# Kernel tuning notes

Hardware: AMD Instinct MI355X
Metric: run time of the kernel (lower is better)

The kernel has to match this reference:

```python
import jax, jax.numpy as jnp
import numpy as np

N0, N1, N2, N3 = 600000, 100000, 10000, 1000
E0, E1, E2 = 1000000, 100000, 10000
DIN, DH, DOUT = 128, 256, 47


def _glorot(k, fan_in, fan_out):
    s = np.sqrt(2.0 / (fan_in + fan_out)).astype(np.float32)
    return jax.random.normal(k, (fan_in, fan_out), jnp.float32) * s


def setup_inputs() -> dict:
    key = jax.random.key(0)
    ks = jax.random.split(key, 13)
    return {
        "x": jax.random.normal(ks[0], (N0, DIN), jnp.float32),
        "src0": jax.random.randint(ks[1], (E0,), 0, N0, jnp.int32),
        "dst0": jax.random.randint(ks[2], (E0,), 0, N1, jnp.int32),
        "src1": jax.random.randint(ks[3], (E1,), 0, N1, jnp.int32),
        "dst1": jax.random.randint(ks[4], (E1,), 0, N2, jnp.int32),
        "src2": jax.random.randint(ks[5], (E2,), 0, N2, jnp.int32),
        "dst2": jax.random.randint(ks[6], (E2,), 0, N3, jnp.int32),
        "Wl0": _glorot(ks[7], DIN, DH), "Wr0": _glorot(ks[8], DIN, DH),
        "b0": jnp.zeros((DH,), jnp.float32),
        "Wl1": _glorot(ks[9], DH, DH), "Wr1": _glorot(ks[10], DH, DH),
        "b1": jnp.zeros((DH,), jnp.float32),
        "Wl2": _glorot(ks[11], DH, DOUT), "Wr2": _glorot(ks[12], DH, DOUT),
        "b2": jnp.zeros((DOUT,), jnp.float32),
        "size1": N1, "size2": N2, "size3": N3,
    }


def _sage_conv(x, src, dst, n_tgt, Wl, Wr, b):
    # PyG SAGEConv (mean aggr, root_weight=True, bias in lin_l) on a bipartite
    # sampled subgraph: x_src = x (all frontier nodes), x_tgt = x[:n_tgt].
    msgs = x[src]                                   # [E, Din] gather
    agg = jax.ops.segment_sum(msgs, dst, num_segments=n_tgt)
    cnt = jax.ops.segment_sum(jnp.ones((dst.shape[0],), x.dtype), dst,
                              num_segments=n_tgt)
    mean = agg / jnp.maximum(cnt, 1.0)[:, None]     # [n_tgt, Din]
    return mean @ Wl + b + x[:n_tgt] @ Wr           # [n_tgt, Dout]


def reference(x, src0, dst0, src1, dst1, src2, dst2,
              Wl0, Wr0, b0, Wl1, Wr1, b1, Wl2, Wr2, b2,
              size1, size2, size3):
    # layer 0
    h = jax.nn.relu(_sage_conv(x, src0, dst0, size1, Wl0, Wr0, b0))
    # dropout(p=0.5) is identity in eval mode
    # layer 1
    h = jax.nn.relu(_sage_conv(h, src1, dst1, size2, Wl1, Wr1, b1))
    # layer 2 (no relu/dropout)
    h = _sage_conv(h, src2, dst2, size3, Wl2, Wr2, b2)
    return jax.nn.log_softmax(h, axis=-1)           # [size3, out_channels]
```

## Files before the change

kernel.cpp:

```cpp
#include <hip/hip_runtime.h>
#include <hip/hip_bf16.h>
#include <cstdint>
#include <cstddef>
#include <cmath>

#define N0C 600000
#define N1C 100000
#define N2C 10000
#define N3C 1000
#define E0C 1000000
#define E1C 100000
#define E2C 10000

typedef unsigned short u16;
typedef unsigned int u32;
typedef __attribute__((ext_vector_type(8))) short bf16x8;
typedef __attribute__((ext_vector_type(4))) float f32x4;

__device__ __forceinline__ u16 f2b(float x) {
  u32 u = __builtin_bit_cast(u32, x);
  u32 r = (u + 0x7fffu + ((u >> 16) & 1u)) >> 16;
  return (u16)r;
}
__device__ __forceinline__ u16 f2b_hw(float x) {
  __hip_bfloat16 h = __float2bfloat16(x);
  u16 r;
  __builtin_memcpy(&r, &h, 2);
  return r;
}
__device__ __forceinline__ float b2f(u16 h) {
  u32 u = ((u32)h) << 16;
  return __builtin_bit_cast(float, u);
}

__global__ __launch_bounds__(256) void hist3(
    const int* __restrict__ d0, const int* __restrict__ d1,
    const int* __restrict__ d2, const int* __restrict__ s1,
    int* __restrict__ c0, int* __restrict__ c1, int* __restrict__ c2,
    int* __restrict__ f) {
  int i = blockIdx.x * blockDim.x + threadIdx.x;
  if (i < E0C) {
    atomicAdd(&c0[d0[i]], 1);
    if (i < N2C) f[i] = 1;
  } else if (i < E0C + E1C) {
    int j = i - E0C;
    atomicAdd(&c1[d1[j]], 1);
    f[s1[j]] = 1;
  } else if (i < E0C + E1C + E2C) {
    atomicAdd(&c2[d2[i - E0C - E1C]], 1);
  }
}

__global__ __launch_bounds__(256) void scan_block3(
    int* __restrict__ c0, int* __restrict__ c1, int* __restrict__ c2,
    int* __restrict__ f, int* __restrict__ p0, int* __restrict__ p1,
    int* __restrict__ p2, int* __restrict__ pf) {
  __shared__ int sdata[256];
  const int b = blockIdx.x;
  int* data; int n; int* partials; int lb;
  if (b < 98)       { data = c0; n = N1C; partials = p0; lb = b; }
  else if (b < 108) { data = c1; n = N2C; partials = p1; lb = b - 98; }
  else if (b < 109) { data = c2; n = N3C; partials = p2; lb = b - 108; }
  else              { data = f;  n = N1C; partials = pf; lb = b - 109; }
  const int t = threadIdx.x;
  const int idx = lb * 1024 + t * 4;
  int v[4];
  int sum = 0;
#pragma unroll
  for (int k = 0; k < 4; k++) {
    int x = (idx + k < n) ? data[idx + k] : 0;
    v[k] = x; sum += x;
  }
  sdata[t] = sum;
  __syncthreads();
  for (int off = 1; off < 256; off <<= 1) {
    int x = (t >= off) ? sdata[t - off] : 0;
    __syncthreads();
    sdata[t] += x;
    __syncthreads();
  }
  int run = (t > 0) ? sdata[t - 1] : 0;
#pragma unroll
  for (int k = 0; k < 4; k++) {
    run += v[k];
    if (idx + k < n) data[idx + k] = run;
  }
  if (t == 255) partials[lb] = sdata[255];
}

__global__ __launch_bounds__(128) void scan_partials3(
    int* __restrict__ p0, int* __restrict__ p1, int* __restrict__ p2,
    int* __restrict__ pf) {
  __shared__ int sdata[128];
  int* p; int nb;
  if (blockIdx.x == 0)      { p = p0; nb = 98; }
  else if (blockIdx.x == 1) { p = p1; nb = 10; }
  else if (blockIdx.x == 2) { p = p2; nb = 1; }
  else                      { p = pf; nb = 98; }
  const int t = threadIdx.x;
  sdata[t] = (t < nb) ? p[t] : 0;
  __syncthreads();
  for (int off = 1; off < 128; off <<= 1) {
    int x = (t >= off) ? sdata[t - off] : 0;
    __syncthreads();
    sdata[t] += x;
    __syncthreads();
  }
  int ex = (t > 0) ? sdata[t - 1] : 0;
  if (t < nb) p[t] = ex;
}

__global__ __launch_bounds__(256) void addoff3(
    const int* __restrict__ c0, const int* __restrict__ c1,
    const int* __restrict__ c2, const int* __restrict__ p0,
    const int* __restrict__ p1, const int* __restrict__ p2,
    int* __restrict__ o0, int* __restrict__ o1, int* __restrict__ o2,
    const int* __restrict__ f, const int* __restrict__ pf,
    int* __restrict__ cidx, int* __restrict__ list,
    int* __restrict__ cnt_need) {
  int i = blockIdx.x * blockDim.x + threadIdx.x;
  if (i < N1C) {
    o0[i + 1] = c0[i] + p0[i >> 10];
    if (i == 0) o0[0] = 0;
    int F = f[i] + pf[i >> 10];
    int prev = (i > 0) ? (f[i - 1] + pf[(i - 1) >> 10]) : 0;
    cidx[i] = prev;
    if (F > prev) list[prev] = i;
    if (i == N1C - 1) cnt_need[0] = F;
  } else if (i < N1C + N2C) {
    int j = i - N1C;
    o1[j + 1] = c1[j] + p1[j >> 10];
    if (j == 0) o1[0] = 0;
  } else if (i < N1C + N2C + N3C) {
    int j = i - N1C - N2C;
    o2[j + 1] = c2[j] + p2[j >> 10];
    if (j == 0) o2[0] = 0;
  }
}

__global__ __launch_bounds__(256) void fill3(
    const int* __restrict__ s0, const int* __restrict__ d0,
    const int* __restrict__ s1, const int* __restrict__ d1,
    const int* __restrict__ s2, const int* __restrict__ d2,
    const int* __restrict__ o0, const int* __restrict__ o1,
    const int* __restrict__ o2, int* __restrict__ u0, int* __restrict__ u1,
    int* __restrict__ u2, int* __restrict__ e0, int* __restrict__ e1,
    int* __restrict__ e2, const int* __restrict__ cidx) {
  int i = blockIdx.x * blockDim.x + threadIdx.x;
  if (i < E0C) {
    int d = d0[i]; int p = atomicAdd(&u0[d], 1); e0[o0[d] + p] = s0[i];
  } else if (i < E0C + E1C) {
    int j = i - E0C;
    int d = d1[j]; int p = atomicAdd(&u1[d], 1);
    e1[o1[d] + p] = cidx[s1[j]];
  } else if (i < E0C + E1C + E2C) {
    int j = i - E0C - E1C;
    int d = d2[j]; int p = atomicAdd(&u2[d], 1); e2[o2[d] + p] = s2[j];
  }
}

__global__ __launch_bounds__(256) void cvt_wt2(
    const float* __restrict__ Wl0, const float* __restrict__ Wr0,
    const float* __restrict__ Wl1, const float* __restrict__ Wr1,
    u16* __restrict__ Wt0, u16* __restrict__ Wt1) {
  int idx = blockIdx.x * blockDim.x + threadIdx.x;
  if (idx < 256 * 256) {
    int n = idx >> 8, k = idx & 255;
    float v = (k < 128) ? Wl0[(size_t)k * 256 + n] : Wr0[(size_t)(k - 128) * 256 + n];
    Wt0[idx] = f2b(v);
  } else if (idx < 256 * 256 + 256 * 512) {
    int j = idx - 256 * 256;
    int n = j >> 9, k = j & 511;
    float v = (k < 256) ? Wl1[(size_t)k * 256 + n] : Wr1[(size_t)(k - 256) * 256 + n];
    Wt1[j] = f2b(v);
  }
}

__global__ __launch_bounds__(256) void gather128_f32(
    const float* __restrict__ X, const int* __restrict__ off,
    const int* __restrict__ esrc, const int* __restrict__ list,
    const int* __restrict__ cnt_need, u16* __restrict__ mean) {
  int w = (blockIdx.x * blockDim.x + threadIdx.x) >> 6;
  int lane = threadIdx.x & 63;
  if (w >= cnt_need[0]) return;
  const int node = list[w];
  const int half = lane >> 5, l32 = lane & 31;
  int s = off[node], e = off[node + 1];
  float a0 = 0.f, a1 = 0.f, a2 = 0.f, a3 = 0.f;
  int j = s;
  for (; j + 3 < e; j += 4) {
    float4 v0 = *(const float4*)(X + (size_t)esrc[j + half] * 128 + l32 * 4);
    float4 v1 = *(const float4*)(X + (size_t)esrc[j + 2 + half] * 128 + l32 * 4);
    a0 += v0.x + v1.x; a1 += v0.y + v1.y;
    a2 += v0.z + v1.z; a3 += v0.w + v1.w;
  }
  for (; j + 1 < e; j += 2) {
    float4 v = *(const float4*)(X + (size_t)esrc[j + half] * 128 + l32 * 4);
    a0 += v.x; a1 += v.y; a2 += v.z; a3 += v.w;
  }
  if (j < e && half == 0) {
    float4 v = *(const float4*)(X + (size_t)esrc[j] * 128 + l32 * 4);
    a0 += v.x; a1 += v.y; a2 += v.z; a3 += v.w;
  }
  a0 += __shfl_xor(a0, 32, 64);
  a1 += __shfl_xor(a1, 32, 64);
  a2 += __shfl_xor(a2, 32, 64);
  a3 += __shfl_xor(a3, 32, 64);
  if (half == 0) {
    float inv = 1.0f / fmaxf((float)(e - s), 1.0f);
    uint2 pk;
    pk.x = ((u32)f2b(a1 * inv) << 16) | (u32)f2b(a0 * inv);
    pk.y = ((u32)f2b(a3 * inv) << 16) | (u32)f2b(a2 * inv);
    *(uint2*)(mean + (size_t)w * 128 + l32 * 4) = pk;
  }
}

__global__ __launch_bounds__(256) void gather256_bf16(
    const u16* __restrict__ X, const int* __restrict__ off,
    const int* __restrict__ esrc, int Nt, u16* __restrict__ mean) {
  int w = (blockIdx.x * blockDim.x + threadIdx.x) >> 6;
  int lane = threadIdx.x & 63;
  if (w >= Nt) return;
  int s = off[w], e = off[w + 1];
  float a0 = 0.f, a1 = 0.f, a2 = 0.f, a3 = 0.f;
  int j = s;
  for (; j + 3 < e; j += 4) {
    ushort4 v0 = *(const ushort4*)(X + (size_t)esrc[j + 0] * 256 + lane * 4);
    ushort4 v1 = *(const ushort4*)(X + (size_t)esrc[j + 1] * 256 + lane * 4);
    ushort4 v2 = *(const ushort4*)(X + (size_t)esrc[j + 2] * 256 + lane * 4);
    ushort4 v3 = *(const ushort4*)(X + (size_t)esrc[j + 3] * 256 + lane * 4);
    a0 += b2f(v0.x) + b2f(v1.x) + b2f(v2.x) + b2f(v3.x);
    a1 += b2f(v0.y) + b2f(v1.y) + b2f(v2.y) + b2f(v3.y);
    a2 += b2f(v0.z) + b2f(v1.z) + b2f(v2.z) + b2f(v3.z);
    a3 += b2f(v0.w) + b2f(v1.w) + b2f(v2.w) + b2f(v3.w);
  }
  for (; j < e; j++) {
    ushort4 v0 = *(const ushort4*)(X + (size_t)esrc[j] * 256 + lane * 4);
    a0 += b2f(v0.x); a1 += b2f(v0.y); a2 += b2f(v0.z); a3 += b2f(v0.w);
  }
  float inv = 1.0f / fmaxf((float)(e - s), 1.0f);
  ushort4 o;
  o.x = f2b(a0 * inv); o.y = f2b(a1 * inv); o.z = f2b(a2 * inv); o.w = f2b(a3 * inv);
  *(ushort4*)(mean + (size_t)w * 256 + lane * 4) = o;
}

__global__ __launch_bounds__(256) void gemm_mfma_l0(
    const u16* __restrict__ A1, const float* __restrict__ A2,
    const int* __restrict__ list, const int* __restrict__ cnt_need,
    const u16* __restrict__ Wt, const float* __restrict__ bias,
    u16* __restrict__ C) {
  const int M = cnt_need[0];
  if ((int)blockIdx.x * 128 >= M) return;
  const int tid = threadIdx.x;
  const int wave = tid >> 6, lane = tid & 63;
  const int lr = lane & 15, quad = lane >> 4;
  const int wr = wave >> 1, wc = wave & 1;
  const int rowBase = blockIdx.x * 128 + wr * 64;
  const int colBase = blockIdx.y * 128 + wc * 64;

  f32x4 acc[4][4] = {};

  int rrow[4], node[4];
#pragma unroll
  for (int mt = 0; mt < 4; mt++) {
    int r = rowBase + mt * 16 + lr;
    if (r >= M) r = M - 1;
    rrow[mt] = r;
    node[mt] = list[r];
  }
  const u16* wrow[4];
  float bs[4];
#pragma unroll
  for (int nt = 0; nt < 4; nt++) {
    int n = colBase + nt * 16 + lr;
    wrow[nt] = Wt + (size_t)n * 256;
    bs[nt] = bias[n];
  }

#pragma unroll
  for (int kt = 0; kt < 128; kt += 32) {
    bf16x8 af[4], bfr[4];
#pragma unroll
    for (int mt = 0; mt < 4; mt++)
      af[mt] = *(const bf16x8*)(A1 + (size_t)rrow[mt] * 128 + kt + quad * 8);
#pragma unroll
    for (int nt = 0; nt < 4; nt++)
      bfr[nt] = *(const bf16x8*)(wrow[nt] + kt + quad * 8);
#pragma unroll
    for (int mt = 0; mt < 4; mt++)
#pragma unroll
      for (int nt = 0; nt < 4; nt++)
        acc[mt][nt] = __builtin_amdgcn_mfma_f32_16x16x32_bf16(
            af[mt], bfr[nt], acc[mt][nt], 0, 0, 0);
  }
#pragma unroll
  for (int kt = 0; kt < 128; kt += 32) {
    bf16x8 af[4], bfr[4];
#pragma unroll
    for (int mt = 0; mt < 4; mt++) {
      const float* s = A2 + (size_t)node[mt] * 128 + kt + quad * 8;
      float4 v0 = *(const float4*)s;
      float4 v1 = *(const float4*)(s + 4);
      bf16x8 t;
      t[0] = (short)f2b_hw(v0.x); t[1] = (short)f2b_hw(v0.y);
      t[2] = (short)f2b_hw(v0.z); t[3] = (short)f2b_hw(v0.w);
      t[4] = (short)f2b_hw(v1.x); t[5] = (short)f2b_hw(v1.y);
      t[6] = (short)f2b_hw(v1.z); t[7] = (short)f2b_hw(v1.w);
      af[mt] = t;
    }
#pragma unroll
    for (int nt = 0; nt < 4; nt++)
      bfr[nt] = *(const bf16x8*)(wrow[nt] + 128 + kt + quad * 8);
#pragma unroll
    for (int mt = 0; mt < 4; mt++)
#pragma unroll
      for (int nt = 0; nt < 4; nt++)
        acc[mt][nt] = __builtin_amdgcn_mfma_f32_16x16x32_bf16(
            af[mt], bfr[nt], acc[mt][nt], 0, 0, 0);
  }

#pragma unroll
  for (int mt = 0; mt < 4; mt++) {
#pragma unroll
    for (int reg = 0; reg < 4; reg++) {
      int row = rowBase + mt * 16 + quad * 4 + reg;
      if (row < M) {
#pragma unroll
        for (int nt = 0; nt < 4; nt++) {
          float v = fmaxf(acc[mt][nt][reg] + bs[nt], 0.f);
          C[(size_t)row * 256 + colBase + nt * 16 + lr] = f2b(v);
        }
      }
    }
  }
}

__global__ __launch_bounds__(256) void gemm_mfma(
    const u16* __restrict__ A1, const u16* __restrict__ A2, int Kh,
    const u16* __restrict__ Wt, const float* __restrict__ bias,
    u16* __restrict__ C, int M, int do_relu) {
  const int tid = threadIdx.x;
  const int wave = tid >> 6, lane = tid & 63;
  const int lr = lane & 15, quad = lane >> 4;
  const int wr = wave >> 1, wc = wave & 1;
  const int rowBase = blockIdx.x * 128 + wr * 64;
  const int colBase = blockIdx.y * 128 + wc * 64;
  const int Ktot = 2 * Kh;

  f32x4 acc[4][4] = {};

  size_t aoff[4];
#pragma unroll
  for (int mt = 0; mt < 4; mt++) {
    int r = rowBase + mt * 16 + lr;
    if (r >= M) r = M - 1;
    aoff[mt] = (size_t)r * Kh;
  }
  const u16* wrow[4];
  float bs[4];
#pragma unroll
  for (int nt = 0; nt < 4; nt++) {
    int n = colBase + nt * 16 + lr;
    wrow[nt] = Wt + (size_t)n * Ktot;
    bs[nt] = bias[n];
  }

#pragma unroll
  for (int half = 0; half < 2; half++) {
    const u16* Asrc = half ? A2 : A1;
    const int kb = half * Kh;
    for (int kt = 0; kt < Kh; kt += 32) {
      bf16x8 af[4], bfr[4];
#pragma unroll
      for (int mt = 0; mt < 4; mt++)
        af[mt] = *(const bf16x8*)(Asrc + aoff[mt] + kt + quad * 8);
#pragma unroll
      for (int nt = 0; nt < 4; nt++)
        bfr[nt] = *(const bf16x8*)(wrow[nt] + kb + kt + quad * 8);
#pragma unroll
      for (int mt = 0; mt < 4; mt++)
#pragma unroll
        for (int nt = 0; nt < 4; nt++)
          acc[mt][nt] = __builtin_amdgcn_mfma_f32_16x16x32_bf16(
              af[mt], bfr[nt], acc[mt][nt], 0, 0, 0);
    }
  }

#pragma unroll
  for (int mt = 0; mt < 4; mt++) {
#pragma unroll
    for (int reg = 0; reg < 4; reg++) {
      int row = rowBase + mt * 16 + quad * 4 + reg;
      if (row < M) {
#pragma unroll
        for (int nt = 0; nt < 4; nt++) {
          float v = acc[mt][nt][reg] + bs[nt];
          if (do_relu) v = fmaxf(v, 0.f);
          C[(size_t)row * 256 + colBase + nt * 16 + lr] = f2b(v);
        }
      }
    }
  }
}

__global__ __launch_bounds__(64) void l2_fused(
    const u16* __restrict__ h2, const int* __restrict__ off,
    const int* __restrict__ esrc, const float* __restrict__ Wl2,
    const float* __restrict__ Wr2, const float* __restrict__ b2,
    float* __restrict__ out) {
  __shared__ float arow[512];
  const int i = blockIdx.x;
  const int lane = threadIdx.x;

  int s = off[i], e = off[i + 1];
  float a0 = 0.f, a1 = 0.f, a2 = 0.f, a3 = 0.f;
  int j = s;
  for (; j + 3 < e; j += 4) {
    ushort4 v0 = *(const ushort4*)(h2 + (size_t)esrc[j + 0] * 256 + lane * 4);
    ushort4 v1 = *(const ushort4*)(h2 + (size_t)esrc[j + 1] * 256 + lane * 4);
    ushort4 v2 = *(const ushort4*)(h2 + (size_t)esrc[j + 2] * 256 + lane * 4);
    ushort4 v3 = *(const ushort4*)(h2 + (size_t)esrc[j + 3] * 256 + lane * 4);
    a0 += b2f(v0.x) + b2f(v1.x) + b2f(v2.x) + b2f(v3.x);
    a1 += b2f(v0.y) + b2f(v1.y) + b2f(v2.y) + b2f(v3.y);
    a2 += b2f(v0.z) + b2f(v1.z) + b2f(v2.z) + b2f(v3.z);
    a3 += b2f(v0.w) + b2f(v1.w) + b2f(v2.w) + b2f(v3.w);
  }
  for (; j < e; j++) {
    ushort4 v0 = *(const ushort4*)(h2 + (size_t)esrc[j] * 256 + lane * 4);
    a0 += b2f(v0.x); a1 += b2f(v0.y); a2 += b2f(v0.z); a3 += b2f(v0.w);
  }
  float inv = 1.0f / fmaxf((float)(e - s), 1.0f);
  arow[lane * 4 + 0] = a0 * inv;
  arow[lane * 4 + 1] = a1 * inv;
  arow[lane * 4 + 2] = a2 * inv;
  arow[lane * 4 + 3] = a3 * inv;
  ushort4 r = *(const ushort4*)(h2 + (size_t)i * 256 + lane * 4);
  arow[256 + lane * 4 + 0] = b2f(r.x);
  arow[256 + lane * 4 + 1] = b2f(r.y);
  arow[256 + lane * 4 + 2] = b2f(r.z);
  arow[256 + lane * 4 + 3] = b2f(r.w);
  __syncthreads();

  float acc = 0.0f;
  if (lane < 47) {
    acc = b2[lane];
#pragma unroll 4
    for (int k = 0; k < 256; k++) acc += arow[k] * Wl2[k * 47 + lane];
#pragma unroll 4
    for (int k = 0; k < 256; k++) acc += arow[256 + k] * Wr2[k * 47 + lane];
  }
  float v = (lane < 47) ? acc : -INFINITY;
#pragma unroll
  for (int off2 = 32; off2 >= 1; off2 >>= 1) v = fmaxf(v, __shfl_xor(v, off2, 64));
  float e2 = (lane < 47) ? expf(acc - v) : 0.0f;
  float s2 = e2;
#pragma unroll
  for (int off2 = 32; off2 >= 1; off2 >>= 1) s2 += __shfl_xor(s2, off2, 64);
  if (lane < 47) out[(size_t)i * 47 + lane] = acc - v - logf(s2);
}

extern "C" void kernel_launch(void* const* d_in, const int* in_sizes, int n_in,
                              void* d_out, int out_size, void* d_ws, size_t ws_size,
                              hipStream_t stream) {
  (void)in_sizes; (void)n_in; (void)out_size; (void)ws_size;
  const float* x   = (const float*)d_in[0];
  const int* src0  = (const int*)d_in[1];
  const int* dst0  = (const int*)d_in[2];
  const int* src1  = (const int*)d_in[3];
  const int* dst1  = (const int*)d_in[4];
  const int* src2  = (const int*)d_in[5];
  const int* dst2  = (const int*)d_in[6];
  const float* Wl0 = (const float*)d_in[7];
  const float* Wr0 = (const float*)d_in[8];
  const float* b0  = (const float*)d_in[9];
  const float* Wl1 = (const float*)d_in[10];
  const float* Wr1 = (const float*)d_in[11];
  const float* b1  = (const float*)d_in[12];
  const float* Wl2 = (const float*)d_in[13];
  const float* Wr2 = (const float*)d_in[14];
  const float* b2  = (const float*)d_in[15];

  char* p = (char*)d_ws;
  u16* mean0 = (u16*)p; p += (size_t)N1C * 128 * 2;
  u16* h1    = (u16*)p; p += (size_t)N1C * 256 * 2;
  u16* mean1 = (u16*)p; p += (size_t)N2C * 256 * 2;
  u16* h2    = (u16*)p; p += (size_t)N2C * 256 * 2;
  u16* Wt0   = (u16*)p; p += (size_t)256 * 256 * 2;
  u16* Wt1   = (u16*)p; p += (size_t)256 * 512 * 2;
  int* cnt0  = (int*)p;
  int* cur0  = cnt0 + 100000;
  int* cnt1  = cur0 + 100000;
  int* cur1  = cnt1 + 10000;
  int* cnt2  = cur1 + 10000;
  int* cur2  = cnt2 + 1000;
  int* f     = cur2 + 1000;
  int* off0  = f + 100000 + 48;
  int* off1  = off0 + 100096;
  int* off2  = off1 + 10112;
  int* part0 = off2 + 1088;
  int* part1 = part0 + 128;
  int* part2 = part1 + 128;
  int* pf    = part2 + 128;
  int* cntN  = pf + 128;
  int* cidx  = cntN + 64;
  int* list  = cidx + 100000;
  int* esrc0 = list + 100000;
  int* esrc1 = esrc0 + 1000000;
  int* esrc2 = esrc1 + 100000;
  float* out = (float*)d_out;

  hipMemsetAsync(cnt0, 0, (size_t)322000 * 4, stream);
  hist3<<<(E0C + E1C + E2C + 255) / 256, 256, 0, stream>>>(
      dst0, dst1, dst2, src1, cnt0, cnt1, cnt2, f);
  scan_block3<<<207, 256, 0, stream>>>(cnt0, cnt1, cnt2, f,
                                       part0, part1, part2, pf);
  scan_partials3<<<4, 128, 0, stream>>>(part0, part1, part2, pf);
  addoff3<<<(N1C + N2C + N3C + 255) / 256, 256, 0, stream>>>(
      cnt0, cnt1, cnt2, part0, part1, part2, off0, off1, off2,
      f, pf, cidx, list, cntN);
  fill3<<<(E0C + E1C + E2C + 255) / 256, 256, 0, stream>>>(
      src0, dst0, src1, dst1, src2, dst2, off0, off1, off2,
      cur0, cur1, cur2, esrc0, esrc1, esrc2, cidx);

  cvt_wt2<<<(256 * 256 + 256 * 512 + 255) / 256, 256, 0, stream>>>(
      Wl0, Wr0, Wl1, Wr1, Wt0, Wt1);

  gather128_f32<<<N1C / 4, 256, 0, stream>>>(x, off0, esrc0, list, cntN, mean0);
  gemm_mfma_l0<<<dim3(782, 2), 256, 0, stream>>>(mean0, x, list, cntN,
                                                 Wt0, b0, h1);

  gather256_bf16<<<N2C / 4, 256, 0, stream>>>(h1, off1, esrc1, N2C, mean1);
  gemm_mfma<<<dim3(79, 2), 256, 0, stream>>>(mean1, h1, 256, Wt1, b1, h2, N2C, 1);

  l2_fused<<<N3C, 64, 0, stream>>>(h2, off2, esrc2, Wl2, Wr2, b2, out);
}
```

Baseline: 696.7 us.

## Fold partial scans into addoff, compact frontier via atomics, merge weight conversion

Removes the scan_partials3 kernel by redoing the small partial-sum scan in shared memory inside addoff3. The frontier-node scan is replaced by an atomic counter that assigns compact ids to needed nodes beyond the first N2C. The weight conversion kernel is merged into fill3, and the layer-0 gather loop is unrolled to 8 edges per iteration. This cuts two kernel launches plus the frontier scan work, at the cost of a nondeterministic compaction order that changes the row order of the mean0 and h1 buffers.

```diff
diff --git a/kernel.cpp b/kernel.cpp
--- a/kernel.cpp
+++ b/kernel.cpp
@@ -37,11 +37,11 @@
     const int* __restrict__ d0, const int* __restrict__ d1,
     const int* __restrict__ d2, const int* __restrict__ s1,
     int* __restrict__ c0, int* __restrict__ c1, int* __restrict__ c2,
-    int* __restrict__ f) {
+    int* __restrict__ f, int* __restrict__ cntN) {
   int i = blockIdx.x * blockDim.x + threadIdx.x;
+  if (i == 0) cntN[0] = N2C;
   if (i < E0C) {
     atomicAdd(&c0[d0[i]], 1);
-    if (i < N2C) f[i] = 1;
   } else if (i < E0C + E1C) {
     int j = i - E0C;
     atomicAdd(&c1[d1[j]], 1);
@@ -53,15 +53,13 @@
 
 __global__ __launch_bounds__(256) void scan_block3(
     int* __restrict__ c0, int* __restrict__ c1, int* __restrict__ c2,
-    int* __restrict__ f, int* __restrict__ p0, int* __restrict__ p1,
-    int* __restrict__ p2, int* __restrict__ pf) {
+    int* __restrict__ p0, int* __restrict__ p1, int* __restrict__ p2) {
   __shared__ int sdata[256];
   const int b = blockIdx.x;
   int* data; int n; int* partials; int lb;
   if (b < 98)       { data = c0; n = N1C; partials = p0; lb = b; }
   else if (b < 108) { data = c1; n = N2C; partials = p1; lb = b - 98; }
-  else if (b < 109) { data = c2; n = N3C; partials = p2; lb = b - 108; }
-  else              { data = f;  n = N1C; partials = pf; lb = b - 109; }
+  else              { data = c2; n = N3C; partials = p2; lb = b - 108; }
   const int t = threadIdx.x;
   const int idx = lb * 1024 + t * 4;
   int v[4];
@@ -88,52 +86,46 @@
   if (t == 255) partials[lb] = sdata[255];
 }
 
-__global__ __launch_bounds__(128) void scan_partials3(
-    int* __restrict__ p0, int* __restrict__ p1, int* __restrict__ p2,
-    int* __restrict__ pf) {
-  __shared__ int sdata[128];
-  int* p; int nb;
-  if (blockIdx.x == 0)      { p = p0; nb = 98; }
-  else if (blockIdx.x == 1) { p = p1; nb = 10; }
-  else if (blockIdx.x == 2) { p = p2; nb = 1; }
-  else                      { p = pf; nb = 98; }
-  const int t = threadIdx.x;
-  sdata[t] = (t < nb) ? p[t] : 0;
-  __syncthreads();
-  for (int off = 1; off < 128; off <<= 1) {
-    int x = (t >= off) ? sdata[t - off] : 0;
-    __syncthreads();
-    sdata[t] += x;
-    __syncthreads();
-  }
-  int ex = (t > 0) ? sdata[t - 1] : 0;
-  if (t < nb) p[t] = ex;
-}
-
 __global__ __launch_bounds__(256) void addoff3(
     const int* __restrict__ c0, const int* __restrict__ c1,
     const int* __restrict__ c2, const int* __restrict__ p0,
-    const int* __restrict__ p1, const int* __restrict__ p2,
+    const int* __restrict__ p1,
     int* __restrict__ o0, int* __restrict__ o1, int* __restrict__ o2,
-    const int* __restrict__ f, const int* __restrict__ pf,
-    int* __restrict__ cidx, int* __restrict__ list,
-    int* __restrict__ cnt_need) {
-  int i = blockIdx.x * blockDim.x + threadIdx.x;
+    const int* __restrict__ f, int* __restrict__ cidx,
+    int* __restrict__ list, int* __restrict__ cntN) {
+  __shared__ int sp0[128];
+  __shared__ int sp1[16];
+  const int t = threadIdx.x;
+  if (t < 128) sp0[t] = (t < 98) ? p0[t] : 0;
+  if (t >= 128 && t < 144) sp1[t - 128] = ((t - 128) < 10) ? p1[t - 128] : 0;
+  __syncthreads();
+  for (int off = 1; off < 128; off <<= 1) {
+    int x0 = (t < 128 && t >= off) ? sp0[t - off] : 0;
+    int x1 = (t >= 128 && t < 144 && (t - 128) >= off) ? sp1[t - 128 - off] : 0;
+    __syncthreads();
+    if (t < 128) sp0[t] += x0;
+    if (t >= 128 && t < 144) sp1[t - 128] += x1;
+    __syncthreads();
+  }
+  int i = blockIdx.x * blockDim.x + t;
   if (i < N1C) {
-    o0[i + 1] = c0[i] + p0[i >> 10];
+    int q = i >> 10;
+    o0[i + 1] = c0[i] + (q ? sp0[q - 1] : 0);
     if (i == 0) o0[0] = 0;
-    int F = f[i] + pf[i >> 10];
-    int prev = (i > 0) ? (f[i - 1] + pf[(i - 1) >> 10]) : 0;
-    cidx[i] = prev;
-    if (F > prev) list[prev] = i;
-    if (i == N1C - 1) cnt_need[0] = F;
+    if (i < N2C) {
+      cidx[i] = i; list[i] = i;
+    } else if (f[i]) {
+      int id = atomicAdd(cntN, 1);
+      cidx[i] = id; list[id] = i;
+    }
   } else if (i < N1C + N2C) {
     int j = i - N1C;
-    o1[j + 1] = c1[j] + p1[j >> 10];
+    int q = j >> 10;
+    o1[j + 1] = c1[j] + (q ? sp1[q - 1] : 0);
     if (j == 0) o1[0] = 0;
   } else if (i < N1C + N2C + N3C) {
     int j = i - N1C - N2C;
-    o2[j + 1] = c2[j] + p2[j >> 10];
+    o2[j + 1] = c2[j];
     if (j == 0) o2[0] = 0;
   }
 }
@@ -145,7 +137,10 @@
     const int* __restrict__ o0, const int* __restrict__ o1,
     const int* __restrict__ o2, int* __restrict__ u0, int* __restrict__ u1,
     int* __restrict__ u2, int* __restrict__ e0, int* __restrict__ e1,
-    int* __restrict__ e2, const int* __restrict__ cidx) {
+    int* __restrict__ e2, const int* __restrict__ cidx,
+    const float* __restrict__ Wl0, const float* __restrict__ Wr0,
+    const float* __restrict__ Wl1, const float* __restrict__ Wr1,
+    u16* __restrict__ Wt0, u16* __restrict__ Wt1) {
   int i = blockIdx.x * blockDim.x + threadIdx.x;
   if (i < E0C) {
     int d = d0[i]; int p = atomicAdd(&u0[d], 1); e0[o0[d] + p] = s0[i];
@@ -156,23 +151,20 @@
   } else if (i < E0C + E1C + E2C) {
     int j = i - E0C - E1C;
     int d = d2[j]; int p = atomicAdd(&u2[d], 1); e2[o2[d] + p] = s2[j];
-  }
-}
-
-__global__ __launch_bounds__(256) void cvt_wt2(
-    const float* __restrict__ Wl0, const float* __restrict__ Wr0,
-    const float* __restrict__ Wl1, const float* __restrict__ Wr1,
-    u16* __restrict__ Wt0, u16* __restrict__ Wt1) {
-  int idx = blockIdx.x * blockDim.x + threadIdx.x;
-  if (idx < 256 * 256) {
-    int n = idx >> 8, k = idx & 255;
-    float v = (k < 128) ? Wl0[(size_t)k * 256 + n] : Wr0[(size_t)(k - 128) * 256 + n];
-    Wt0[idx] = f2b(v);
-  } else if (idx < 256 * 256 + 256 * 512) {
-    int j = idx - 256 * 256;
-    int n = j >> 9, k = j & 511;
-    float v = (k < 256) ? Wl1[(size_t)k * 256 + n] : Wr1[(size_t)(k - 256) * 256 + n];
-    Wt1[j] = f2b(v);
+  } else {
+    int k = i - (E0C + E1C + E2C);
+    if (k < 256 * 256) {
+      int n = k >> 8, kk = k & 255;
+      float v = (kk < 128) ? Wl0[(size_t)kk * 256 + n]
+                           : Wr0[(size_t)(kk - 128) * 256 + n];
+      Wt0[k] = f2b(v);
+    } else if (k < 256 * 256 + 256 * 512) {
+      int j = k - 256 * 256;
+      int n = j >> 9, kk = j & 511;
+      float v = (kk < 256) ? Wl1[(size_t)kk * 256 + n]
+                           : Wr1[(size_t)(kk - 256) * 256 + n];
+      Wt1[j] = f2b(v);
+    }
   }
 }
 
@@ -188,11 +180,15 @@
   int s = off[node], e = off[node + 1];
   float a0 = 0.f, a1 = 0.f, a2 = 0.f, a3 = 0.f;
   int j = s;
-  for (; j + 3 < e; j += 4) {
+  for (; j + 7 < e; j += 8) {
     float4 v0 = *(const float4*)(X + (size_t)esrc[j + half] * 128 + l32 * 4);
     float4 v1 = *(const float4*)(X + (size_t)esrc[j + 2 + half] * 128 + l32 * 4);
-    a0 += v0.x + v1.x; a1 += v0.y + v1.y;
-    a2 += v0.z + v1.z; a3 += v0.w + v1.w;
+    float4 v2 = *(const float4*)(X + (size_t)esrc[j + 4 + half] * 128 + l32 * 4);
+    float4 v3 = *(const float4*)(X + (size_t)esrc[j + 6 + half] * 128 + l32 * 4);
+    a0 += v0.x + v1.x + v2.x + v3.x;
+    a1 += v0.y + v1.y + v2.y + v3.y;
+    a2 += v0.z + v1.z + v2.z + v3.z;
+    a3 += v0.w + v1.w + v2.w + v3.w;
   }
   for (; j + 1 < e; j += 2) {
     float4 v = *(const float4*)(X + (size_t)esrc[j + half] * 128 + l32 * 4);
@@ -500,8 +496,7 @@
   int* part0 = off2 + 1088;
   int* part1 = part0 + 128;
   int* part2 = part1 + 128;
-  int* pf    = part2 + 128;
-  int* cntN  = pf + 128;
+  int* cntN  = part2 + 128;
   int* cidx  = cntN + 64;
   int* list  = cidx + 100000;
   int* esrc0 = list + 100000;
@@ -511,18 +506,15 @@
 
   hipMemsetAsync(cnt0, 0, (size_t)322000 * 4, stream);
   hist3<<<(E0C + E1C + E2C + 255) / 256, 256, 0, stream>>>(
-      dst0, dst1, dst2, src1, cnt0, cnt1, cnt2, f);
-  scan_block3<<<207, 256, 0, stream>>>(cnt0, cnt1, cnt2, f,
-                                       part0, part1, part2, pf);
-  scan_partials3<<<4, 128, 0, stream>>>(part0, part1, part2, pf);
+      dst0, dst1, dst2, src1, cnt0, cnt1, cnt2, f, cntN);
+  scan_block3<<<109, 256, 0, stream>>>(cnt0, cnt1, cnt2, part0, part1, part2);
   addoff3<<<(N1C + N2C + N3C + 255) / 256, 256, 0, stream>>>(
-      cnt0, cnt1, cnt2, part0, part1, part2, off0, off1, off2,
-      f, pf, cidx, list, cntN);
-  fill3<<<(E0C + E1C + E2C + 255) / 256, 256, 0, stream>>>(
+      cnt0, cnt1, cnt2, part0, part1, off0, off1, off2,
+      f, cidx, list, cntN);
+  fill3<<<(E0C + E1C + E2C + 256 * 256 + 256 * 512 + 255) / 256, 256, 0,
+         stream>>>(
       src0, dst0, src1, dst1, src2, dst2, off0, off1, off2,
-      cur0, cur1, cur2, esrc0, esrc1, esrc2, cidx);
-
-  cvt_wt2<<<(256 * 256 + 256 * 512 + 255) / 256, 256, 0, stream>>>(
+      cur0, cur1, cur2, esrc0, esrc1, esrc2, cidx,
       Wl0, Wr0, Wl1, Wr1, Wt0, Wt1);
 
   gather128_f32<<<N1C / 4, 256, 0, stream>>>(x, off0, esrc0, list, cntN, mean0);
```

Result: no change. 699.2 us (+0.4%).
